# Kernel tuning notes

Hardware: AMD Instinct MI355X
Metric: run time of the kernel (lower is better)

Reference implementation:

```python
import jax, jax.numpy as jnp
import numpy as np

NEG_SLOPE = 0.2  # LeakyReLU slope
B, F_BAND, T = 32, 128, 2048
HID, NCLASS = 256, 64


def _corrcoef(m):
    # m: [..., n, k] -> correlation matrix between rows, [..., n, n] (torch.corrcoef semantics)
    m = m - m.mean(axis=-1, keepdims=True)
    c = jnp.einsum('...ik,...jk->...ij', m, m)
    d = jnp.sqrt(jnp.clip(jnp.diagonal(c, axis1=-2, axis2=-1), 0.0, None))
    corr = c / (d[..., :, None] * d[..., None, :])
    return jnp.clip(corr, -1.0, 1.0)


def _leaky(x):
    return jnp.where(x >= 0, x, NEG_SLOPE * x)


def setup_inputs() -> dict:
    key = jax.random.key(0)
    ks = jax.random.split(key, 9)
    def lin(k, fin, fout):
        return jax.random.normal(k, (fin, fout), dtype=jnp.float32) / np.sqrt(fin)
    x = jax.random.normal(ks[0], (B, F_BAND, T), dtype=jnp.float32)
    return {
        'x': x,
        'W1': lin(ks[1], T, HID),      'b1': jnp.zeros((HID,), jnp.float32),
        'W2': lin(ks[2], HID, HID),    'b2': jnp.zeros((HID,), jnp.float32),
        'W3': lin(ks[3], HID, NCLASS), 'b3': jnp.zeros((NCLASS,), jnp.float32),
        'W4': lin(ks[4], NCLASS, NCLASS), 'b4': jnp.zeros((NCLASS,), jnp.float32),
    }


def reference(x, W1, b1, W2, b2, W3, b3, W4, b4):
    Bs, Fb, Tt = x.shape
    node = Fb
    step = node  # typeFeature=2 -> overlap=0
    A = len(range(0, Tt - node, step))  # number of time windows
    # windows: x[:, :, a*node:(a+1)*node] -> [B, A, F, node]
    xw = x[:, :, :A * node].reshape(Bs, Fb, A, node).transpose(0, 2, 1, 3)
    # torch.corrcoef(fi.T): rows = window-column index (node), variables over F bands
    adj = _corrcoef(jnp.swapaxes(xw, -1, -2))  # [B, A, node, node] == [B, A, F, F]
    adj = jnp.nan_to_num((adj + 1.0) * 0.5)
    # gnnBlock vectorized over all A windows (x broadcast along A). Dropout is eval-mode no-op.
    h = _leaky(jnp.einsum('banm,bmt->bant', adj, x) @ W1 + b1)    # [B,A,F,HID]
    h = _leaky(jnp.einsum('banm,bamh->banh', adj, h) @ W2 + b2)   # [B,A,F,HID]
    xa = _leaky(jnp.einsum('banm,bamh->banh', adj, h) @ W3 + b3)  # [B,A,F,C]
    # typeFeature==2 head: mean over nodes, corrcoef over windows, gc4
    xa = xa.mean(axis=2)         # [B, A, C]
    adj2 = _corrcoef(xa)         # [B, A, A]
    out = _leaky(jnp.einsum('bij,bjc->bic', adj2, xa) @ W4 + b4)  # [B, A, C]
    # max over dim=1; GradMultiply with grad_mul=1.0 is identity in fwd
    return out.max(axis=1)       # [B, C]
```

## Files before the change

### kernel.cpp

```cpp
#include <hip/hip_runtime.h>


typedef float f32x4 __attribute__((ext_vector_type(4)));
typedef __bf16 bf16x8 __attribute__((ext_vector_type(8)));
typedef unsigned short u16x4 __attribute__((ext_vector_type(4)));
typedef unsigned short u16x8 __attribute__((ext_vector_type(8)));

__device__ inline unsigned short f2b(float f) {
  unsigned int u = __float_as_uint(f);
  unsigned int r = u + 0x7fffu + ((u >> 16) & 1u);
  return (unsigned short)(r >> 16);
}
__device__ inline float leaky(float v) { return v >= 0.f ? v : 0.2f * v; }

#define SWZ(k, r) ((k) ^ (((r) & 7) << 3))

__global__ __launch_bounds__(256) void k_prep(const float* __restrict__ x,
                                              const float* __restrict__ W1,
                                              const float* __restrict__ W2,
                                              const float* __restrict__ W3,
                                              unsigned short* __restrict__ W1T,
                                              unsigned short* __restrict__ W2T,
                                              unsigned short* __restrict__ W3T,
                                              unsigned short* __restrict__ xT) {
  __shared__ float t[64][65];
  const int bid = blockIdx.x;
  const int tid = threadIdx.x;
  if (bid < 148) {
    const float* src;
    unsigned short* dst;
    int K, N, k0, n0;
    if (bid < 128) {
      src = W1; dst = W1T; K = 2048; N = 256;
      k0 = (bid >> 2) * 64; n0 = (bid & 3) * 64;
    } else if (bid < 144) {
      src = W2; dst = W2T; K = 256; N = 256;
      int i = bid - 128; k0 = (i >> 2) * 64; n0 = (i & 3) * 64;
    } else {
      src = W3; dst = W3T; K = 256; N = 64;
      int i = bid - 144; k0 = i * 64; n0 = 0;
    }
#pragma unroll
    for (int it = 0; it < 16; ++it) {
      int e = tid + it * 256, r = e >> 6, c = e & 63;
      t[r][c] = src[(size_t)(k0 + r) * N + n0 + c];
    }
    __syncthreads();
#pragma unroll
    for (int it = 0; it < 16; ++it) {
      int e = tid + it * 256, rr = e >> 6, cc = e & 63;
      dst[(size_t)(n0 + rr) * K + k0 + cc] = f2b(t[cc][rr]);
    }
  } else {
    int idx = bid - 148;
    int b = idx >> 6, rem = idx & 63;
    int tt = rem >> 1, ft = rem & 1;
    int t0 = tt * 64, f0 = ft * 64;
    const float* xb = x + ((size_t)b * 128 + f0) * 2048 + t0;
#pragma unroll
    for (int it = 0; it < 16; ++it) {
      int e = tid + it * 256, r = e >> 6, c = e & 63;
      t[r][c] = xb[(size_t)r * 2048 + c];
    }
    __syncthreads();
    unsigned short* dst = xT + ((size_t)b * 2048 + t0) * 128 + f0;
#pragma unroll
    for (int it = 0; it < 4; ++it) {
      int e = tid + it * 256, rr = e >> 4, c4 = (e & 15) * 4;
      u16x4 s;
#pragma unroll
      for (int q = 0; q < 4; ++q) s[q] = f2b(t[c4 + q][rr]);
      *(u16x4*)&dst[rr * 128 + c4] = s;
    }
  }
}

__global__ __launch_bounds__(512) void k_xw1(const float* __restrict__ x,
                                             const unsigned short* __restrict__ W1T,
                                             unsigned short* __restrict__ XW1T) {
  __shared__ __align__(16) unsigned short sX[2][64 * 64];
  const int tid = threadIdx.x;
  const int w = tid >> 6, lane = tid & 63;
  const int l15 = lane & 15, l4 = lane >> 4;
  const int bx = blockIdx.x;
  const int hid0 = (bx >> 1) * 64, f0 = (bx & 1) * 64;
  const int b = blockIdx.y;
  const float* xb = x + ((size_t)b * 128 + f0) * 2048;
  const int arow = hid0 + (w & 3) * 16 + l15;
  const int nb = (w >> 2) * 32;
  const int fr = tid >> 3, k8 = (tid & 7) * 8;

  f32x4 xr0, xr1;
  f32x4 acc[2] = {};

  auto LOADX = [&](int kb) {
    xr0 = *(const f32x4*)&xb[(size_t)fr * 2048 + kb * 64 + k8];
    xr1 = *(const f32x4*)&xb[(size_t)fr * 2048 + kb * 64 + k8 + 4];
  };
  auto STOREX = [&](int buf) {
    u16x8 s;
#pragma unroll
    for (int j = 0; j < 8; ++j) s[j] = f2b(j < 4 ? xr0[j] : xr1[j - 4]);
    *(u16x8*)&sX[buf][fr * 64 + SWZ(k8, fr)] = s;
  };

  LOADX(0);
  STOREX(0);
  __syncthreads();
  for (int kb = 0; kb < 32; ++kb) {
    if (kb < 31) LOADX(kb + 1);
    const int buf = kb & 1;
    bf16x8 af0 = *(const bf16x8*)&W1T[(size_t)arow * 2048 + kb * 64 + l4 * 8];
    bf16x8 af1 = *(const bf16x8*)&W1T[(size_t)arow * 2048 + kb * 64 + 32 + l4 * 8];
#pragma unroll
    for (int nt = 0; nt < 2; ++nt) {
      int br = nb + nt * 16 + l15;
      bf16x8 b0 = *(const bf16x8*)&sX[buf][br * 64 + SWZ(l4 * 8, br)];
      acc[nt] = __builtin_amdgcn_mfma_f32_16x16x32_bf16(af0, b0, acc[nt], 0, 0, 0);
    }
#pragma unroll
    for (int nt = 0; nt < 2; ++nt) {
      int br = nb + nt * 16 + l15;
      bf16x8 b1 = *(const bf16x8*)&sX[buf][br * 64 + SWZ(32 + l4 * 8, br)];
      acc[nt] = __builtin_amdgcn_mfma_f32_16x16x32_bf16(af1, b1, acc[nt], 0, 0, 0);
    }
    if (kb < 31) {
      STOREX(buf ^ 1);
      __syncthreads();
    }
  }
  unsigned short* dst = XW1T + (size_t)b * 256 * 128;
#pragma unroll
  for (int nt = 0; nt < 2; ++nt)
#pragma unroll
    for (int r = 0; r < 4; ++r) {
      int p = hid0 + (w & 3) * 16 + l4 * 4 + r;
      int f = f0 + nb + nt * 16 + l15;
      dst[p * 128 + f] = f2b(acc[nt][r]);
    }
}

__global__ __launch_bounds__(512) void k_chain(
    const unsigned short* __restrict__ xT, const unsigned short* __restrict__ XW1T,
    const unsigned short* __restrict__ W2T, const unsigned short* __restrict__ W3T,
    const float* __restrict__ b1g, const float* __restrict__ b2g,
    const float* __restrict__ b3g, float* __restrict__ gXa) {
  __shared__ __align__(16) unsigned short R0[128 * 128];
  __shared__ __align__(16) unsigned short R1[128 * 128];
  __shared__ float fS[256];

  const int tid = threadIdx.x;
  const int w = tid >> 6, lane = tid & 63;
  const int l15 = lane & 15, l4 = lane >> 4;
  const int ridx = (blockIdx.x & 7) * 60 + (blockIdx.x >> 3);
  const int b = ridx / 15, a = ridx % 15;
  const int m0 = w * 16;
  const unsigned short* XWb = XW1T + (size_t)b * 256 * 128;
  const float inv128 = 1.f / 128.f;

  const unsigned short* src = xT + ((size_t)b * 2048 + (size_t)a * 128) * 128;
#pragma unroll 1
  for (int it = 0; it < 4; ++it) {
    int tt = tid + it * 512;
    int j = tt >> 4, f8 = (tt & 15) * 8;
    *(u16x8*)&R1[j * 128 + SWZ(f8, j)] = *(const u16x8*)&src[j * 128 + f8];
  }
  __syncthreads();

  bf16x8 afw[4];
#pragma unroll
  for (int ks = 0; ks < 4; ++ks) {
    int ar = m0 + l15;
    afw[ks] = *(const bf16x8*)&R1[ar * 128 + SWZ(ks * 32 + l4 * 8, ar)];
  }
  bf16x8 ones;
#pragma unroll
  for (int q = 0; q < 8; ++q) ones[q] = (__bf16)1.0f;
  f32x4 sacc = {}, dacc = {};
#pragma unroll
  for (int ks = 0; ks < 4; ++ks) {
    sacc = __builtin_amdgcn_mfma_f32_16x16x32_bf16(afw[ks], ones, sacc, 0, 0, 0);
    dacc = __builtin_amdgcn_mfma_f32_16x16x32_bf16(afw[ks], afw[ks], dacc, 0, 0, 0);
  }
#pragma unroll
  for (int r = 0; r < 4; ++r) {
    if (l15 == 0) fS[m0 + l4 * 4 + r] = sacc[r];
    if (l15 == l4 * 4 + r)
      fS[128 + m0 + l4 * 4 + r] = dacc[r] - sacc[r] * sacc[r] * inv128;
  }
  __syncthreads();

  float div[4];
#pragma unroll
  for (int r = 0; r < 4; ++r) {
    float d = fS[128 + m0 + l4 * 4 + r];
    div[r] = d > 0.f ? __frsqrt_rn(d) : 0.f;
  }
#pragma unroll 1
  for (int nt = 0; nt < 8; ++nt) {
    int col = nt * 16 + l15;
    f32x4 c = {};
#pragma unroll
    for (int ks = 0; ks < 4; ++ks) {
      bf16x8 bf = *(const bf16x8*)&R1[col * 128 + SWZ(ks * 32 + l4 * 8, col)];
      c = __builtin_amdgcn_mfma_f32_16x16x32_bf16(afw[ks], bf, c, 0, 0, 0);
    }
    float fc = fS[col];
    float dc = fS[128 + col];
    float djv = dc > 0.f ? __frsqrt_rn(dc) : 0.f;
    u16x4 pk;
#pragma unroll
    for (int r = 0; r < 4; ++r) {
      float v = (c[r] - sacc[r] * fc * inv128) * div[r] * djv;
      v = fminf(1.f, fmaxf(-1.f, v));
      v = 0.5f * v + 0.5f;
      if (div[r] == 0.f || djv == 0.f) v = 0.f;
      pk[r] = f2b(v);
    }
    *(u16x4*)&R0[col * 128 + SWZ(m0 + l4 * 4, col)] = pk;
  }
  __syncthreads();

  bf16x8 afj[4];
#pragma unroll
  for (int ks = 0; ks < 4; ++ks)
    afj[ks] = *(const bf16x8*)&R0[(m0 + l15) * 128 + SWZ(ks * 32 + l4 * 8, m0 + l15)];

#pragma unroll 1
  for (int half = 0; half < 2; ++half) {
    unsigned short* Rd = half ? R0 : R1;
    const unsigned short* Bbase = &XWb[(size_t)half * 128 * 128 + l4 * 8];
    bf16x8 bpf[4];
#pragma unroll
    for (int ks = 0; ks < 4; ++ks)
      bpf[ks] = *(const bf16x8*)&Bbase[(size_t)l15 * 128 + ks * 32];
#pragma unroll 1
    for (int nt = 0; nt < 8; ++nt) {
      bf16x8 bc[4];
#pragma unroll
      for (int ks = 0; ks < 4; ++ks) bc[ks] = bpf[ks];
      if (nt < 7) {
#pragma unroll
        for (int ks = 0; ks < 4; ++ks)
          bpf[ks] = *(const bf16x8*)&Bbase[(size_t)((nt + 1) * 16 + l15) * 128 + ks * 32];
      }
      f32x4 acc = {};
#pragma unroll
      for (int ks = 0; ks < 4; ++ks)
        acc = __builtin_amdgcn_mfma_f32_16x16x32_bf16(afj[ks], bc[ks], acc, 0, 0, 0);
      float bias = b1g[half * 128 + nt * 16 + l15];
#pragma unroll
      for (int r = 0; r < 4; ++r) {
        int row = m0 + l4 * 4 + r;
        Rd[row * 128 + SWZ(nt * 16 + l15, row)] = f2b(leaky(acc[r] + bias));
      }
    }
  }
  __syncthreads();

  f32x4 u2[2][8] = {};
  {
    const unsigned short* A0 = &W2T[(size_t)(w * 32 + l15) * 256 + l4 * 8];
    const unsigned short* A1 = &W2T[(size_t)(w * 32 + 16 + l15) * 256 + l4 * 8];
    bf16x8 a0p = *(const bf16x8*)&A0[0];
    bf16x8 a1p = *(const bf16x8*)&A1[0];
#pragma unroll 1
    for (int ks = 0; ks < 8; ++ks) {
      bf16x8 a0 = a0p, a1 = a1p;
      if (ks < 7) {
        a0p = *(const bf16x8*)&A0[(ks + 1) * 32];
        a1p = *(const bf16x8*)&A1[(ks + 1) * 32];
      }
      const unsigned short* Rs = (ks < 4) ? R1 : R0;
      int kk = (ks & 3) * 32 + l4 * 8;
#pragma unroll
      for (int nt = 0; nt < 8; ++nt) {
        int br = nt * 16 + l15;
        bf16x8 bf = *(const bf16x8*)&Rs[br * 128 + SWZ(kk, br)];
        u2[0][nt] = __builtin_amdgcn_mfma_f32_16x16x32_bf16(a0, bf, u2[0][nt], 0, 0, 0);
        u2[1][nt] = __builtin_amdgcn_mfma_f32_16x16x32_bf16(a1, bf, u2[1][nt], 0, 0, 0);
      }
    }
  }
  __syncthreads();

#pragma unroll
  for (int mt = 0; mt < 2; ++mt)
#pragma unroll
    for (int nt = 0; nt < 8; ++nt)
#pragma unroll
      for (int r = 0; r < 4; ++r) {
        int grow = w * 32 + mt * 16 + l4 * 4 + r;
        int col = nt * 16 + l15;
        unsigned short* Rd = (grow < 128) ? R0 : R1;
        int lr = grow & 127;
        Rd[lr * 128 + SWZ(col, lr)] = f2b(u2[mt][nt][r]);
      }
  __syncthreads();

  f32x4 h2acc[16];
#pragma unroll
  for (int nt = 0; nt < 16; ++nt) h2acc[nt] = f32x4{0.f, 0.f, 0.f, 0.f};
#pragma unroll
  for (int ks = 0; ks < 4; ++ks)
#pragma unroll
    for (int nt = 0; nt < 16; ++nt) {
      int brl = (nt & 7) * 16 + l15;
      const unsigned short* Rs = (nt < 8) ? R0 : R1;
      bf16x8 bf = *(const bf16x8*)&Rs[brl * 128 + SWZ(ks * 32 + l4 * 8, brl)];
      h2acc[nt] = __builtin_amdgcn_mfma_f32_16x16x32_bf16(afj[ks], bf, h2acc[nt], 0, 0, 0);
    }
  __syncthreads();

#pragma unroll
  for (int nt = 0; nt < 16; ++nt) {
    float bias = b2g[nt * 16 + l15];
#pragma unroll
    for (int r = 0; r < 4; ++r) {
      int row = m0 + l4 * 4 + r;
      int coll = (nt & 7) * 16 + l15;
      unsigned short* Rd = (nt < 8) ? R0 : R1;
      Rd[row * 128 + SWZ(coll, row)] = f2b(leaky(h2acc[nt][r] + bias));
    }
  }
  const int mrow = (w >> 1) * 16, ntb = (w & 1) * 4;
  bf16x8 a3f[8];
#pragma unroll
  for (int ks = 0; ks < 8; ++ks)
    a3f[ks] = *(const bf16x8*)&W3T[(size_t)(mrow + l15) * 256 + ks * 32 + l4 * 8];
  __syncthreads();

  f32x4 u3[4] = {};
#pragma unroll
  for (int kh = 0; kh < 2; ++kh) {
    const unsigned short* Rs = kh ? R1 : R0;
#pragma unroll
    for (int ks = 0; ks < 4; ++ks) {
#pragma unroll
      for (int nti = 0; nti < 4; ++nti) {
        int br = (ntb + nti) * 16 + l15;
        bf16x8 bf = *(const bf16x8*)&Rs[br * 128 + SWZ(ks * 32 + l4 * 8, br)];
        u3[nti] = __builtin_amdgcn_mfma_f32_16x16x32_bf16(a3f[kh * 4 + ks], bf, u3[nti], 0, 0, 0);
      }
    }
  }
  __syncthreads();

#pragma unroll
  for (int nti = 0; nti < 4; ++nti)
#pragma unroll
    for (int r = 0; r < 4; ++r) {
      int grow = mrow + l4 * 4 + r;
      int col = (ntb + nti) * 16 + l15;
      R0[grow * 128 + SWZ(col, grow)] = f2b(u3[nti][r]);
    }
  __syncthreads();

  {
    float* pf = reinterpret_cast<float*>(R1);
#pragma unroll 1
    for (int nt = 0; nt < 4; ++nt) {
      f32x4 acc = {};
      int br = nt * 16 + l15;
#pragma unroll
      for (int ks = 0; ks < 4; ++ks) {
        bf16x8 bf = *(const bf16x8*)&R0[br * 128 + SWZ(ks * 32 + l4 * 8, br)];
        acc = __builtin_amdgcn_mfma_f32_16x16x32_bf16(afj[ks], bf, acc, 0, 0, 0);
      }
      float bias = b3g[br];
      float v = 0.f;
#pragma unroll
      for (int r = 0; r < 4; ++r) v += leaky(acc[r] + bias);
      v += __shfl_xor(v, 16);
      v += __shfl_xor(v, 32);
      if (l4 == 0) pf[w * 64 + br] = v;
    }
  }
  __syncthreads();
  if (tid < 64) {
    const float* pf = reinterpret_cast<const float*>(R1);
    float s = 0.f;
#pragma unroll
    for (int gg = 0; gg < 8; ++gg) s += pf[gg * 64 + tid];
    gXa[((size_t)b * 15 + a) * 64 + tid] = s * (1.f / 128.f);
  }
}

__global__ __launch_bounds__(256) void k_head(const float* __restrict__ gXa,
                                              const float* __restrict__ W4,
                                              const float* __restrict__ b4,
                                              float* __restrict__ out) {
  __shared__ float xb[15 * 64];
  __shared__ float c2[15 * 16];
  __shared__ float mu[15];
  __shared__ float dinv[15];
  __shared__ float yy[15 * 64];
  __shared__ float zz[15 * 64];
  const int b = blockIdx.x;
  const int tid = threadIdx.x;
  for (int e = tid; e < 960; e += 256) xb[e] = gXa[(size_t)b * 960 + e];
  __syncthreads();
  if (tid < 15) {
    float s = 0.f;
    for (int c = 0; c < 64; ++c) s += xb[tid * 64 + c];
    mu[tid] = s * (1.f / 64.f);
  }
  __syncthreads();
  if (tid < 225) {
    int p = tid / 15, q = tid % 15;
    float s = 0.f;
    for (int c = 0; c < 64; ++c)
      s += (xb[p * 64 + c] - mu[p]) * (xb[q * 64 + c] - mu[q]);
    c2[p * 16 + q] = s;
  }
  __syncthreads();
  if (tid < 15) {
    float d = c2[tid * 16 + tid];
    dinv[tid] = d > 0.f ? (1.f / sqrtf(d)) : 0.f;
  }
  __syncthreads();
  if (tid < 225) {
    int p = tid / 15, q = tid % 15;
    float v = c2[p * 16 + q] * dinv[p] * dinv[q];
    v = fminf(1.f, fmaxf(-1.f, v));
    if (dinv[p] == 0.f || dinv[q] == 0.f) v = 0.f;
    c2[p * 16 + q] = v;
  }
  __syncthreads();
  for (int e = tid; e < 960; e += 256) {
    int p = e >> 6, c = e & 63;
    float s = 0.f;
    for (int q = 0; q < 15; ++q) s += c2[p * 16 + q] * xb[q * 64 + c];
    yy[e] = s;
  }
  __syncthreads();
  for (int e = tid; e < 960; e += 256) {
    int p = e >> 6, c = e & 63;
    float s = b4[c];
    for (int k = 0; k < 64; ++k) s += yy[p * 64 + k] * W4[k * 64 + c];
    zz[e] = leaky(s);
  }
  __syncthreads();
  if (tid < 64) {
    float m = -INFINITY;
    for (int p = 0; p < 15; ++p) m = fmaxf(m, zz[p * 64 + tid]);
    out[(size_t)b * 64 + tid] = m;
  }
}

extern "C" void kernel_launch(void* const* d_in, const int* in_sizes, int n_in,
                              void* d_out, int out_size, void* d_ws, size_t ws_size,
                              hipStream_t stream) {
  const float* x  = (const float*)d_in[0];
  const float* W1 = (const float*)d_in[1];
  const float* b1 = (const float*)d_in[2];
  const float* W2 = (const float*)d_in[3];
  const float* b2 = (const float*)d_in[4];
  const float* W3 = (const float*)d_in[5];
  const float* b3 = (const float*)d_in[6];
  const float* W4 = (const float*)d_in[7];
  const float* b4 = (const float*)d_in[8];
  float* out = (float*)d_out;

  char* ws = (char*)d_ws;
  unsigned short* xT   = (unsigned short*)ws;
  unsigned short* XW1T = (unsigned short*)(ws + 16777216);
  unsigned short* W1T  = (unsigned short*)(ws + 18874368);
  unsigned short* W2T  = (unsigned short*)(ws + 19922944);
  unsigned short* W3T  = (unsigned short*)(ws + 20054016);
  float* gXa           = (float*)(ws + 20086784);

  k_prep<<<2196, 256, 0, stream>>>(x, W1, W2, W3, W1T, W2T, W3T, xT);
  dim3 gx(8, 32);
  k_xw1<<<gx, 512, 0, stream>>>(x, W1T, XW1T);
  k_chain<<<480, 512, 0, stream>>>(xT, XW1T, W2T, W3T, b1, b2, b3, gXa);
  k_head<<<32, 256, 0, stream>>>(gXa, W4, b4, out);
}
```

Baseline: 118.6 us.

## Merge prep and XW1 kernels, fold head into chain via last-block counter

Combines the weight/x transpose-prep and the x·W1 GEMM into one k_front launch. The GEMM now reads fp32 W1 directly and converts it to bf16 in LDS each k-step, so the W1T workspace pass is gone. The head kernel is folded into k_chain: each batch's last-finishing block (atomic counter) computes the corrcoef/gc4/max head. This cuts launches from four to two and removes one global round-trip of W1. The cost is two extra LDS barriers per k-step in the GEMM, and a counter reset inside k_front that relies on stream ordering.

Result: slower. 167.6 us (+41.3%).

```diff
diff --git a/kernel.cpp b/kernel.cpp
--- a/kernel.cpp
+++ b/kernel.cpp
@@ -15,139 +15,137 @@
 
 #define SWZ(k, r) ((k) ^ (((r) & 7) << 3))
 
-__global__ __launch_bounds__(256) void k_prep(const float* __restrict__ x,
-                                              const float* __restrict__ W1,
-                                              const float* __restrict__ W2,
-                                              const float* __restrict__ W3,
-                                              unsigned short* __restrict__ W1T,
-                                              unsigned short* __restrict__ W2T,
-                                              unsigned short* __restrict__ W3T,
-                                              unsigned short* __restrict__ xT) {
-  __shared__ float t[64][65];
-  const int bid = blockIdx.x;
-  const int tid = threadIdx.x;
-  if (bid < 148) {
+__global__ __launch_bounds__(512) void k_front(const float* __restrict__ x,
+                                               const float* __restrict__ W1,
+                                               const float* __restrict__ W2,
+                                               const float* __restrict__ W3,
+                                               unsigned short* __restrict__ W2T,
+                                               unsigned short* __restrict__ W3T,
+                                               unsigned short* __restrict__ xT,
+                                               unsigned short* __restrict__ XW1T,
+                                               int* __restrict__ cnt) {
+  __shared__ __align__(16) char lds[16640 + 8192 + 16384];
+  float (*tW)[65] = reinterpret_cast<float (*)[65]>(lds);
+  unsigned short* sW = reinterpret_cast<unsigned short*>(lds + 16640);
+  unsigned short (*sX)[64 * 64] =
+      reinterpret_cast<unsigned short (*)[64 * 64]>(lds + 16640 + 8192);
+  const int bid = blockIdx.x, tid = threadIdx.x;
+  const int r = tid >> 3, c8 = (tid & 7) * 8;
+
+  if (bid == 0 && tid < 32) cnt[tid] = 0;
+
+  if (bid < 20) {
     const float* src;
     unsigned short* dst;
     int K, N, k0, n0;
-    if (bid < 128) {
-      src = W1; dst = W1T; K = 2048; N = 256;
-      k0 = (bid >> 2) * 64; n0 = (bid & 3) * 64;
-    } else if (bid < 144) {
-      src = W2; dst = W2T; K = 256; N = 256;
-      int i = bid - 128; k0 = (i >> 2) * 64; n0 = (i & 3) * 64;
-    } else {
-      src = W3; dst = W3T; K = 256; N = 64;
-      int i = bid - 144; k0 = i * 64; n0 = 0;
-    }
-#pragma unroll
-    for (int it = 0; it < 16; ++it) {
-      int e = tid + it * 256, r = e >> 6, c = e & 63;
-      t[r][c] = src[(size_t)(k0 + r) * N + n0 + c];
-    }
-    __syncthreads();
-#pragma unroll
-    for (int it = 0; it < 16; ++it) {
-      int e = tid + it * 256, rr = e >> 6, cc = e & 63;
-      dst[(size_t)(n0 + rr) * K + k0 + cc] = f2b(t[cc][rr]);
-    }
+    if (bid < 16) { src = W2; dst = W2T; K = 256; N = 256; k0 = (bid >> 2) * 64; n0 = (bid & 3) * 64; }
+    else          { src = W3; dst = W3T; K = 256; N = 64;  k0 = (bid - 16) * 64; n0 = 0; }
+#pragma unroll
+    for (int j = 0; j < 8; ++j) tW[r][c8 + j] = src[(size_t)(k0 + r) * N + n0 + c8 + j];
+    __syncthreads();
+    u16x8 s;
+#pragma unroll
+    for (int j = 0; j < 8; ++j) s[j] = f2b(tW[c8 + j][r]);
+    *(u16x8*)&dst[(size_t)(n0 + r) * K + k0 + c8] = s;
+  } else if (bid < 276) {
+    const int i = bid - 20;
+    const int b = i >> 3, q = i & 7;
+    const int hid0 = (q >> 1) * 64, f0 = (q & 1) * 64;
+    const int w = tid >> 6, lane = tid & 63;
+    const int l15 = lane & 15, l4 = lane >> 4;
+    const float* xb = x + ((size_t)b * 128 + f0) * 2048;
+    f32x4 xr0, xr1, wr0, wr1;
+    f32x4 acc[2] = {};
+
+    auto LOADX = [&](int kb) {
+      xr0 = *(const f32x4*)&xb[(size_t)r * 2048 + kb * 64 + c8];
+      xr1 = *(const f32x4*)&xb[(size_t)r * 2048 + kb * 64 + c8 + 4];
+    };
+    auto LOADW = [&](int kb) {
+      wr0 = *(const f32x4*)&W1[(size_t)(kb * 64 + r) * 256 + hid0 + c8];
+      wr1 = *(const f32x4*)&W1[(size_t)(kb * 64 + r) * 256 + hid0 + c8 + 4];
+    };
+    auto STOREX = [&](int buf) {
+      u16x8 s;
+#pragma unroll
+      for (int j = 0; j < 8; ++j) s[j] = f2b(j < 4 ? xr0[j] : xr1[j - 4]);
+      *(u16x8*)&sX[buf][r * 64 + SWZ(c8, r)] = s;
+    };
+    auto STOREW = [&]() {
+#pragma unroll
+      for (int j = 0; j < 4; ++j) { tW[r][c8 + j] = wr0[j]; tW[r][c8 + 4 + j] = wr1[j]; }
+    };
+    auto PACKW = [&]() {
+      u16x8 s;
+#pragma unroll
+      for (int j = 0; j < 8; ++j) s[j] = f2b(tW[c8 + j][r]);
+      *(u16x8*)&sW[r * 64 + SWZ(c8, r)] = s;
+    };
+
+    LOADX(0); LOADW(0);
+    STOREX(0); STOREW();
+    __syncthreads();
+    PACKW();
+    __syncthreads();
+    for (int kb = 0; kb < 32; ++kb) {
+      if (kb < 31) { LOADX(kb + 1); LOADW(kb + 1); }
+      const int buf = kb & 1;
+#pragma unroll
+      for (int ks = 0; ks < 2; ++ks) {
+        int ar = (w & 3) * 16 + l15;
+        bf16x8 af = *(const bf16x8*)&sW[ar * 64 + SWZ(ks * 32 + l4 * 8, ar)];
+#pragma unroll
+        for (int nt = 0; nt < 2; ++nt) {
+          int br = (w >> 2) * 32 + nt * 16 + l15;
+          bf16x8 bf = *(const bf16x8*)&sX[buf][br * 64 + SWZ(ks * 32 + l4 * 8, br)];
+          acc[nt] = __builtin_amdgcn_mfma_f32_16x16x32_bf16(af, bf, acc[nt], 0, 0, 0);
+        }
+      }
+      if (kb < 31) {
+        STOREX(buf ^ 1);
+        STOREW();
+        __syncthreads();
+        PACKW();
+        __syncthreads();
+      }
+    }
+    unsigned short* dst = XW1T + (size_t)b * 256 * 128;
+#pragma unroll
+    for (int nt = 0; nt < 2; ++nt)
+#pragma unroll
+      for (int rr = 0; rr < 4; ++rr) {
+        int p = hid0 + (w & 3) * 16 + l4 * 4 + rr;
+        int f = f0 + (w >> 2) * 32 + nt * 16 + l15;
+        dst[p * 128 + f] = f2b(acc[nt][rr]);
+      }
   } else {
-    int idx = bid - 148;
-    int b = idx >> 6, rem = idx & 63;
-    int tt = rem >> 1, ft = rem & 1;
-    int t0 = tt * 64, f0 = ft * 64;
+    const int i = bid - 276;
+    const int b = i >> 6, rem = i & 63;
+    const int t0 = (rem >> 1) * 64, f0 = (rem & 1) * 64;
     const float* xb = x + ((size_t)b * 128 + f0) * 2048 + t0;
-#pragma unroll
-    for (int it = 0; it < 16; ++it) {
-      int e = tid + it * 256, r = e >> 6, c = e & 63;
-      t[r][c] = xb[(size_t)r * 2048 + c];
-    }
-    __syncthreads();
-    unsigned short* dst = xT + ((size_t)b * 2048 + t0) * 128 + f0;
-#pragma unroll
-    for (int it = 0; it < 4; ++it) {
-      int e = tid + it * 256, rr = e >> 4, c4 = (e & 15) * 4;
-      u16x4 s;
-#pragma unroll
-      for (int q = 0; q < 4; ++q) s[q] = f2b(t[c4 + q][rr]);
-      *(u16x4*)&dst[rr * 128 + c4] = s;
-    }
-  }
-}
-
-__global__ __launch_bounds__(512) void k_xw1(const float* __restrict__ x,
-                                             const unsigned short* __restrict__ W1T,
-                                             unsigned short* __restrict__ XW1T) {
-  __shared__ __align__(16) unsigned short sX[2][64 * 64];
-  const int tid = threadIdx.x;
-  const int w = tid >> 6, lane = tid & 63;
-  const int l15 = lane & 15, l4 = lane >> 4;
-  const int bx = blockIdx.x;
-  const int hid0 = (bx >> 1) * 64, f0 = (bx & 1) * 64;
-  const int b = blockIdx.y;
-  const float* xb = x + ((size_t)b * 128 + f0) * 2048;
-  const int arow = hid0 + (w & 3) * 16 + l15;
-  const int nb = (w >> 2) * 32;
-  const int fr = tid >> 3, k8 = (tid & 7) * 8;
-
-  f32x4 xr0, xr1;
-  f32x4 acc[2] = {};
-
-  auto LOADX = [&](int kb) {
-    xr0 = *(const f32x4*)&xb[(size_t)fr * 2048 + kb * 64 + k8];
-    xr1 = *(const f32x4*)&xb[(size_t)fr * 2048 + kb * 64 + k8 + 4];
-  };
-  auto STOREX = [&](int buf) {
+    f32x4 v0 = *(const f32x4*)&xb[(size_t)r * 2048 + c8];
+    f32x4 v1 = *(const f32x4*)&xb[(size_t)r * 2048 + c8 + 4];
+#pragma unroll
+    for (int j = 0; j < 4; ++j) { tW[r][c8 + j] = v0[j]; tW[r][c8 + 4 + j] = v1[j]; }
+    __syncthreads();
     u16x8 s;
 #pragma unroll
-    for (int j = 0; j < 8; ++j) s[j] = f2b(j < 4 ? xr0[j] : xr1[j - 4]);
-    *(u16x8*)&sX[buf][fr * 64 + SWZ(k8, fr)] = s;
-  };
-
-  LOADX(0);
-  STOREX(0);
-  __syncthreads();
-  for (int kb = 0; kb < 32; ++kb) {
-    if (kb < 31) LOADX(kb + 1);
-    const int buf = kb & 1;
-    bf16x8 af0 = *(const bf16x8*)&W1T[(size_t)arow * 2048 + kb * 64 + l4 * 8];
-    bf16x8 af1 = *(const bf16x8*)&W1T[(size_t)arow * 2048 + kb * 64 + 32 + l4 * 8];
-#pragma unroll
-    for (int nt = 0; nt < 2; ++nt) {
-      int br = nb + nt * 16 + l15;
-      bf16x8 b0 = *(const bf16x8*)&sX[buf][br * 64 + SWZ(l4 * 8, br)];
-      acc[nt] = __builtin_amdgcn_mfma_f32_16x16x32_bf16(af0, b0, acc[nt], 0, 0, 0);
-    }
-#pragma unroll
-    for (int nt = 0; nt < 2; ++nt) {
-      int br = nb + nt * 16 + l15;
-      bf16x8 b1 = *(const bf16x8*)&sX[buf][br * 64 + SWZ(32 + l4 * 8, br)];
-      acc[nt] = __builtin_amdgcn_mfma_f32_16x16x32_bf16(af1, b1, acc[nt], 0, 0, 0);
-    }
-    if (kb < 31) {
-      STOREX(buf ^ 1);
-      __syncthreads();
-    }
-  }
-  unsigned short* dst = XW1T + (size_t)b * 256 * 128;
-#pragma unroll
-  for (int nt = 0; nt < 2; ++nt)
-#pragma unroll
-    for (int r = 0; r < 4; ++r) {
-      int p = hid0 + (w & 3) * 16 + l4 * 4 + r;
-      int f = f0 + nb + nt * 16 + l15;
-      dst[p * 128 + f] = f2b(acc[nt][r]);
-    }
+    for (int j = 0; j < 8; ++j) s[j] = f2b(tW[c8 + j][r]);
+    *(u16x8*)&xT[((size_t)b * 2048 + t0 + r) * 128 + f0 + c8] = s;
+  }
 }
 
 __global__ __launch_bounds__(512) void k_chain(
     const unsigned short* __restrict__ xT, const unsigned short* __restrict__ XW1T,
     const unsigned short* __restrict__ W2T, const unsigned short* __restrict__ W3T,
     const float* __restrict__ b1g, const float* __restrict__ b2g,
-    const float* __restrict__ b3g, float* __restrict__ gXa) {
+    const float* __restrict__ b3g, float* __restrict__ gXa,
+    const float* __restrict__ W4, const float* __restrict__ b4g,
+    float* __restrict__ out, int* __restrict__ cnt) {
   __shared__ __align__(16) unsigned short R0[128 * 128];
   __shared__ __align__(16) unsigned short R1[128 * 128];
   __shared__ float fS[256];
+  __shared__ int sOld;
 
   const int tid = threadIdx.x;
   const int w = tid >> 6, lane = tid & 63;
@@ -175,7 +173,7 @@
   }
   bf16x8 ones;
 #pragma unroll
-  for (int q = 0; q < 8; ++q) ones[q] = (__bf16)1.0f;
+  for (int qq = 0; qq < 8; ++qq) ones[qq] = (__bf16)1.0f;
   f32x4 sacc = {}, dacc = {};
 #pragma unroll
   for (int ks = 0; ks < 4; ++ks) {
@@ -183,18 +181,18 @@
     dacc = __builtin_amdgcn_mfma_f32_16x16x32_bf16(afw[ks], afw[ks], dacc, 0, 0, 0);
   }
 #pragma unroll
-  for (int r = 0; r < 4; ++r) {
-    if (l15 == 0) fS[m0 + l4 * 4 + r] = sacc[r];
-    if (l15 == l4 * 4 + r)
-      fS[128 + m0 + l4 * 4 + r] = dacc[r] - sacc[r] * sacc[r] * inv128;
+  for (int rr = 0; rr < 4; ++rr) {
+    if (l15 == 0) fS[m0 + l4 * 4 + rr] = sacc[rr];
+    if (l15 == l4 * 4 + rr)
+      fS[128 + m0 + l4 * 4 + rr] = dacc[rr] - sacc[rr] * sacc[rr] * inv128;
   }
   __syncthreads();
 
   float div[4];
 #pragma unroll
-  for (int r = 0; r < 4; ++r) {
-    float d = fS[128 + m0 + l4 * 4 + r];
-    div[r] = d > 0.f ? __frsqrt_rn(d) : 0.f;
+  for (int rr = 0; rr < 4; ++rr) {
+    float d = fS[128 + m0 + l4 * 4 + rr];
+    div[rr] = d > 0.f ? __frsqrt_rn(d) : 0.f;
   }
 #pragma unroll 1
   for (int nt = 0; nt < 8; ++nt) {
@@ -210,12 +208,12 @@
     float djv = dc > 0.f ? __frsqrt_rn(dc) : 0.f;
     u16x4 pk;
 #pragma unroll
-    for (int r = 0; r < 4; ++r) {
-      float v = (c[r] - sacc[r] * fc * inv128) * div[r] * djv;
+    for (int rr = 0; rr < 4; ++rr) {
+      float v = (c[rr] - sacc[rr] * fc * inv128) * div[rr] * djv;
       v = fminf(1.f, fmaxf(-1.f, v));
       v = 0.5f * v + 0.5f;
-      if (div[r] == 0.f || djv == 0.f) v = 0.f;
-      pk[r] = f2b(v);
+      if (div[rr] == 0.f || djv == 0.f) v = 0.f;
+      pk[rr] = f2b(v);
     }
     *(u16x4*)&R0[col * 128 + SWZ(m0 + l4 * 4, col)] = pk;
   }
@@ -250,9 +248,9 @@
         acc = __builtin_amdgcn_mfma_f32_16x16x32_bf16(afj[ks], bc[ks], acc, 0, 0, 0);
       float bias = b1g[half * 128 + nt * 16 + l15];
 #pragma unroll
-      for (int r = 0; r < 4; ++r) {
-        int row = m0 + l4 * 4 + r;
-        Rd[row * 128 + SWZ(nt * 16 + l15, row)] = f2b(leaky(acc[r] + bias));
+      for (int rr = 0; rr < 4; ++rr) {
+        int row = m0 + l4 * 4 + rr;
+        Rd[row * 128 + SWZ(nt * 16 + l15, row)] = f2b(leaky(acc[rr] + bias));
       }
     }
   }
@@ -289,12 +287,12 @@
 #pragma unroll
     for (int nt = 0; nt < 8; ++nt)
 #pragma unroll
-      for (int r = 0; r < 4; ++r) {
-        int grow = w * 32 + mt * 16 + l4 * 4 + r;
+      for (int rr = 0; rr < 4; ++rr) {
+        int grow = w * 32 + mt * 16 + l4 * 4 + rr;
         int col = nt * 16 + l15;
         unsigned short* Rd = (grow < 128) ? R0 : R1;
         int lr = grow & 127;
-        Rd[lr * 128 + SWZ(col, lr)] = f2b(u2[mt][nt][r]);
+        Rd[lr * 128 + SWZ(col, lr)] = f2b(u2[mt][nt][rr]);
       }
   __syncthreads();
 
@@ -316,11 +314,11 @@
   for (int nt = 0; nt < 16; ++nt) {
     float bias = b2g[nt * 16 + l15];
 #pragma unroll
-    for (int r = 0; r < 4; ++r) {
-      int row = m0 + l4 * 4 + r;
+    for (int rr = 0; rr < 4; ++rr) {
+      int row = m0 + l4 * 4 + rr;
       int coll = (nt & 7) * 16 + l15;
       unsigned short* Rd = (nt < 8) ? R0 : R1;
-      Rd[row * 128 + SWZ(coll, row)] = f2b(leaky(h2acc[nt][r] + bias));
+      Rd[row * 128 + SWZ(coll, row)] = f2b(leaky(h2acc[nt][rr] + bias));
     }
   }
   const int mrow = (w >> 1) * 16, ntb = (w & 1) * 4;
@@ -349,10 +347,10 @@
 #pragma unroll
   for (int nti = 0; nti < 4; ++nti)
 #pragma unroll
-    for (int r = 0; r < 4; ++r) {
-      int grow = mrow + l4 * 4 + r;
+    for (int rr = 0; rr < 4; ++rr) {
+      int grow = mrow + l4 * 4 + rr;
       int col = (ntb + nti) * 16 + l15;
-      R0[grow * 128 + SWZ(col, grow)] = f2b(u3[nti][r]);
+      R0[grow * 128 + SWZ(col, grow)] = f2b(u3[nti][rr]);
     }
   __syncthreads();
 
@@ -370,7 +368,7 @@
       float bias = b3g[br];
       float v = 0.f;
 #pragma unroll
-      for (int r = 0; r < 4; ++r) v += leaky(acc[r] + bias);
+      for (int rr = 0; rr < 4; ++rr) v += leaky(acc[rr] + bias);
       v += __shfl_xor(v, 16);
       v += __shfl_xor(v, 32);
       if (l4 == 0) pf[w * 64 + br] = v;
@@ -384,67 +382,66 @@
     for (int gg = 0; gg < 8; ++gg) s += pf[gg * 64 + tid];
     gXa[((size_t)b * 15 + a) * 64 + tid] = s * (1.f / 128.f);
   }
-}
-
-__global__ __launch_bounds__(256) void k_head(const float* __restrict__ gXa,
-                                              const float* __restrict__ W4,
-                                              const float* __restrict__ b4,
-                                              float* __restrict__ out) {
-  __shared__ float xb[15 * 64];
-  __shared__ float c2[15 * 16];
-  __shared__ float mu[15];
-  __shared__ float dinv[15];
-  __shared__ float yy[15 * 64];
-  __shared__ float zz[15 * 64];
-  const int b = blockIdx.x;
-  const int tid = threadIdx.x;
-  for (int e = tid; e < 960; e += 256) xb[e] = gXa[(size_t)b * 960 + e];
-  __syncthreads();
-  if (tid < 15) {
-    float s = 0.f;
-    for (int c = 0; c < 64; ++c) s += xb[tid * 64 + c];
-    mu[tid] = s * (1.f / 64.f);
-  }
-  __syncthreads();
-  if (tid < 225) {
-    int p = tid / 15, q = tid % 15;
-    float s = 0.f;
-    for (int c = 0; c < 64; ++c)
-      s += (xb[p * 64 + c] - mu[p]) * (xb[q * 64 + c] - mu[q]);
-    c2[p * 16 + q] = s;
-  }
-  __syncthreads();
-  if (tid < 15) {
-    float d = c2[tid * 16 + tid];
-    dinv[tid] = d > 0.f ? (1.f / sqrtf(d)) : 0.f;
-  }
-  __syncthreads();
-  if (tid < 225) {
-    int p = tid / 15, q = tid % 15;
-    float v = c2[p * 16 + q] * dinv[p] * dinv[q];
-    v = fminf(1.f, fmaxf(-1.f, v));
-    if (dinv[p] == 0.f || dinv[q] == 0.f) v = 0.f;
-    c2[p * 16 + q] = v;
-  }
-  __syncthreads();
-  for (int e = tid; e < 960; e += 256) {
-    int p = e >> 6, c = e & 63;
-    float s = 0.f;
-    for (int q = 0; q < 15; ++q) s += c2[p * 16 + q] * xb[q * 64 + c];
-    yy[e] = s;
-  }
-  __syncthreads();
-  for (int e = tid; e < 960; e += 256) {
-    int p = e >> 6, c = e & 63;
-    float s = b4[c];
-    for (int k = 0; k < 64; ++k) s += yy[p * 64 + k] * W4[k * 64 + c];
-    zz[e] = leaky(s);
-  }
-  __syncthreads();
-  if (tid < 64) {
-    float m = -INFINITY;
-    for (int p = 0; p < 15; ++p) m = fmaxf(m, zz[p * 64 + tid]);
-    out[(size_t)b * 64 + tid] = m;
+
+  __threadfence();
+  if (tid == 0) sOld = atomicAdd(&cnt[b], 1);
+  __syncthreads();
+  if (sOld == 14) {
+    __threadfence();
+    float* hxb = reinterpret_cast<float*>(R0);
+    float* hc2 = hxb + 960;
+    float* hmu = hc2 + 256;
+    float* hdv = hmu + 16;
+    float* hyy = reinterpret_cast<float*>(R1);
+    float* hzz = hyy + 960;
+    for (int e = tid; e < 960; e += 512) hxb[e] = gXa[(size_t)b * 960 + e];
+    __syncthreads();
+    if (tid < 15) {
+      float s = 0.f;
+      for (int c = 0; c < 64; ++c) s += hxb[tid * 64 + c];
+      hmu[tid] = s * (1.f / 64.f);
+    }
+    __syncthreads();
+    if (tid < 225) {
+      int p = tid / 15, qq = tid % 15;
+      float s = 0.f;
+      for (int c = 0; c < 64; ++c)
+        s += (hxb[p * 64 + c] - hmu[p]) * (hxb[qq * 64 + c] - hmu[qq]);
+      hc2[p * 16 + qq] = s;
+    }
+    __syncthreads();
+    if (tid < 15) {
+      float d = hc2[tid * 16 + tid];
+      hdv[tid] = d > 0.f ? (1.f / sqrtf(d)) : 0.f;
+    }
+    __syncthreads();
+    if (tid < 225) {
+      int p = tid / 15, qq = tid % 15;
+      float v = hc2[p * 16 + qq] * hdv[p] * hdv[qq];
+      v = fminf(1.f, fmaxf(-1.f, v));
+      if (hdv[p] == 0.f || hdv[qq] == 0.f) v = 0.f;
+      hc2[p * 16 + qq] = v;
+    }
+    __syncthreads();
+    for (int e = tid; e < 960; e += 512) {
+      int p = e >> 6, c = e & 63;
+      float s = 0.f;
+      for (int qq = 0; qq < 15; ++qq) s += hc2[p * 16 + qq] * hxb[qq * 64 + c];
+      hyy[e] = s;
+    }
+    __syncthreads();
+    for (int e = tid; e < 960; e += 512) {
+      int p = e >> 6, c = e & 63;
+      float s = b4g[c];
+      for (int k = 0; k < 64; ++k) s += hyy[p * 64 + k] * W4[k * 64 + c];
+      hzz[e] = leaky(s);
+    }
+    __syncthreads();
+    if (tid < 64) {
+      float m = -INFINITY;
+      for (int p = 0; p < 15; ++p) m = fmaxf(m, hzz[p * 64 + tid]);
+      out[(size_t)b * 64 + tid] = m;
+    }
   }
 }
 
@@ -465,14 +462,12 @@
   char* ws = (char*)d_ws;
   unsigned short* xT   = (unsigned short*)ws;
   unsigned short* XW1T = (unsigned short*)(ws + 16777216);
-  unsigned short* W1T  = (unsigned short*)(ws + 18874368);
-  unsigned short* W2T  = (unsigned short*)(ws + 19922944);
-  unsigned short* W3T  = (unsigned short*)(ws + 20054016);
-  float* gXa           = (float*)(ws + 20086784);
-
-  k_prep<<<2196, 256, 0, stream>>>(x, W1, W2, W3, W1T, W2T, W3T, xT);
-  dim3 gx(8, 32);
-  k_xw1<<<gx, 512, 0, stream>>>(x, W1T, XW1T);
-  k_chain<<<480, 512, 0, stream>>>(xT, XW1T, W2T, W3T, b1, b2, b3, gXa);
-  k_head<<<32, 256, 0, stream>>>(gXa, W4, b4, out);
+  unsigned short* W2T  = (unsigned short*)(ws + 18874368);
+  unsigned short* W3T  = (unsigned short*)(ws + 19005440);
+  float* gXa           = (float*)(ws + 19038208);
+  int* cnt             = (int*)(ws + 19161088);
+
+  k_front<<<2324, 512, 0, stream>>>(x, W1, W2, W3, W2T, W3T, xT, XW1T, cnt);
+  k_chain<<<480, 512, 0, stream>>>(xT, XW1T, W2T, W3T, b1, b2, b3, gXa,
+                                   W4, b4, out, cnt);
 }
```
